# Optimization experiments

Measured on AMD Instinct MI355X. Metric: run time of the kernel, lower is better.

## Reference

```python
import jax, jax.numpy as jnp
import numpy as np

EPS = 1e-6  # cell eps
LN_EPS = 1e-5  # torch LayerNorm default


def layer_norm(x, gamma, beta):
    mu = jnp.mean(x, axis=-1, keepdims=True)
    var = jnp.mean(jnp.square(x - mu), axis=-1, keepdims=True)
    return (x - mu) * jax.lax.rsqrt(var + LN_EPS) * gamma + beta


def normalized_exp_gate(pre):
    centered = pre - jnp.mean(pre, axis=1, keepdims=True)
    e = jnp.exp(jnp.clip(centered, -5.0, 5.0))
    return e / (jnp.sum(e, axis=1, keepdims=True) + EPS)


def setup_inputs() -> dict:
    key = jax.random.key(0)
    B, Din, H = 8192, 512, 1024
    ks = jax.random.split(key, 16)
    std = 1.0 / np.sqrt(H)
    u = lambda k, shape: jax.random.uniform(k, shape, jnp.float32, -std, std)
    return {
        "x": jax.random.normal(ks[0], (B, Din), jnp.float32),
        "h_prev": jax.random.normal(ks[1], (B, H), jnp.float32),
        "c_prev": jax.random.normal(ks[2], (B, H), jnp.float32),
        "Wx": u(ks[3], (4 * H, Din)),
        "bx": u(ks[4], (4 * H,)),
        "Wh": u(ks[5], (4 * H, H)),
        "bh": u(ks[6], (4 * H,)),
        "ln_in_g": u(ks[7], (4 * H,)),
        "ln_in_b": u(ks[8], (4 * H,)),
        "ln_hu_g": u(ks[9], (4 * H,)),
        "ln_hu_b": u(ks[10], (4 * H,)),
        "ln_c_g": u(ks[11], (H,)),
        "ln_c_b": u(ks[12], (H,)),
        "ln_h_g": u(ks[13], (H,)),
        "ln_h_b": u(ks[14], (H,)),
    }


def reference(x, h_prev, c_prev, Wx, bx, Wh, bh,
              ln_in_g, ln_in_b, ln_hu_g, ln_hu_b,
              ln_c_g, ln_c_b, ln_h_g, ln_h_b):
    # dropout p=0 -> identity (eval mode)
    gates_x = layer_norm(x @ Wx.T + bx, ln_in_g, ln_in_b)      # [B, 4H]
    gates_h = layer_norm(h_prev @ Wh.T + bh, ln_hu_g, ln_hu_b)  # [B, 4H]
    gates = gates_x + gates_h
    i, f, g, o = jnp.split(gates, 4, axis=1)
    i = normalized_exp_gate(i)
    f = normalized_exp_gate(f)
    gate_sum = i + f
    i = i / (gate_sum + EPS)
    f = f / (gate_sum + EPS)
    c_tilde = jnp.tanh(g)
    c = layer_norm(f * c_prev + i * c_tilde, ln_c_g, ln_c_b)
    o = jax.nn.sigmoid(o)
    c_out = layer_norm(jnp.tanh(c), ln_h_g, ln_h_b)
    h = o * c_out
    return (h, c)
```

## Files before the change

### kernel.cpp

```cpp
#include <hip/hip_runtime.h>
#include <hip/hip_bf16.h>
#include <stdint.h>
#include <math.h>

#define EPS_CELL 1e-6f
#define LN_EPS   1e-5f

typedef short short8 __attribute__((ext_vector_type(8)));
typedef float f32x4 __attribute__((ext_vector_type(4)));
typedef unsigned short ushort;

__device__ __forceinline__ ushort f2bf(float f) {
    union { float f; uint32_t u; } v; v.f = f;
    uint32_t r = v.u + 0x7FFFu + ((v.u >> 16) & 1u);
    return (ushort)(r >> 16);
}
__device__ __forceinline__ float bfbits2f(uint32_t hi16_in_place) {
    union { uint32_t u; float f; } v; v.u = hi16_in_place;
    return v.f;
}

__device__ __forceinline__ float fexp(float x)  { return __builtin_amdgcn_exp2f(x * 1.4426950408889634f); }
__device__ __forceinline__ float frcp(float x)  { return __builtin_amdgcn_rcpf(x); }
__device__ __forceinline__ float frsq(float x)  { return __builtin_amdgcn_rsqf(x); }
__device__ __forceinline__ float ftanh(float x) {
    float xc = fminf(fmaxf(x, -15.f), 15.f);
    float t  = fexp(2.f * xc);
    return (t - 1.f) * frcp(t + 1.f);
}
__device__ __forceinline__ float fsigm(float x) { return frcp(1.f + fexp(-x)); }

__global__ __launch_bounds__(256) void cast_f32_bf16(const float* __restrict__ in,
                                                     ushort* __restrict__ out,
                                                     int n) {
    int i = (blockIdx.x * 256 + threadIdx.x) * 8;
    if (i >= n) return;
    const float4* p = (const float4*)(in + i);
    float4 a = p[0], b = p[1];
    uint4 r;
    r.x = (uint32_t)f2bf(a.x) | ((uint32_t)f2bf(a.y) << 16);
    r.y = (uint32_t)f2bf(a.z) | ((uint32_t)f2bf(a.w) << 16);
    r.z = (uint32_t)f2bf(b.x) | ((uint32_t)f2bf(b.y) << 16);
    r.w = (uint32_t)f2bf(b.z) | ((uint32_t)f2bf(b.w) << 16);
    *(uint4*)(out + i) = r;
}

#define BAR()        __builtin_amdgcn_s_barrier()
#define SPRIO(x)     __builtin_amdgcn_s_setprio(x)
#define WAIT_LGKM0() do { asm volatile("s_waitcnt lgkmcnt(0)" ::: "memory"); \
                          __builtin_amdgcn_sched_barrier(0); } while (0)
#define WAIT_VM4()   do { asm volatile("s_waitcnt vmcnt(4)" ::: "memory"); \
                          __builtin_amdgcn_sched_barrier(0); } while (0)
#define WAIT_VM0()   do { asm volatile("s_waitcnt vmcnt(0)" ::: "memory"); \
                          __builtin_amdgcn_sched_barrier(0); } while (0)

template<int K>
__global__ __launch_bounds__(512, 2) void gemm256_8ph(
        const ushort* __restrict__ Ag,
        const ushort* __restrict__ Bg,
        const float*  __restrict__ bias,
        ushort* __restrict__ C,
        int M, int GN) {
    constexpr int NT = K / 64;
    constexpr int NP = NT / 2;

    __shared__ ushort lds[65536];

    const int t    = threadIdx.x;
    const int lane = t & 63;
    const int w    = t >> 6;
    const int wr   = w >> 2;
    const int wc   = w & 3;
    const int ln   = lane & 15;
    const int hi   = lane >> 4;
    const int sx   = ln & 7;

    const int bid = blockIdx.x;
    const int wg  = (bid & 7) * 64 + (bid >> 3);
    const int n0  = (wg & 15) * 256;
    const int m0  = (wg >> 4) * 256;

    const int trow = t >> 3;
    const int scol = (((t & 7) ^ (trow & 7)) * 8);

#define STG_A(buf, j, kb) __builtin_amdgcn_global_load_lds( \
    (const __attribute__((address_space(1))) void*)(Ag + (size_t)(m0 + (j)*64 + trow) * K + (kb) + scol), \
    (__attribute__((address_space(3))) void*)(lds + (buf)*32768 + (j)*4096 + t*8), 16, 0, 0)
#define STG_B(buf, j, kb) __builtin_amdgcn_global_load_lds( \
    (const __attribute__((address_space(1))) void*)(Bg + (size_t)(n0 + (j)*64 + trow) * K + (kb) + scol), \
    (__attribute__((address_space(3))) void*)(lds + (buf)*32768 + 16384 + (j)*4096 + t*8), 16, 0, 0)

    const int ca0  = ((0 + hi) ^ sx) * 8;
    const int ca1  = ((4 + hi) ^ sx) * 8;
    const int arow = (wr * 128 + ln) * 64;
    const int brow = (wc * 64 + ln) * 64;

    short8 af[2][4], bf0[2][2], bf1[2][2];
    f32x4  acc[8][4] = {};

#define LD_A(buf, mbase) do { _Pragma("unroll") for (int m = 0; m < 4; ++m) { \
    af[0][m] = *(const short8*)&lds[(buf)*32768 + arow + ((mbase)+m)*1024 + ca0]; \
    af[1][m] = *(const short8*)&lds[(buf)*32768 + arow + ((mbase)+m)*1024 + ca1]; } } while (0)
#define LD_B(dst, buf, nbase) do { _Pragma("unroll") for (int n = 0; n < 2; ++n) { \
    dst[0][n] = *(const short8*)&lds[(buf)*32768 + 16384 + brow + ((nbase)+n)*1024 + ca0]; \
    dst[1][n] = *(const short8*)&lds[(buf)*32768 + 16384 + brow + ((nbase)+n)*1024 + ca1]; } } while (0)
#define MMQ(mb, nb, B_) do { _Pragma("unroll") for (int kk = 0; kk < 2; ++kk) \
    _Pragma("unroll") for (int m = 0; m < 4; ++m) \
    _Pragma("unroll") for (int n = 0; n < 2; ++n) \
        acc[(mb)+m][(nb)+n] = __builtin_amdgcn_mfma_f32_16x16x32_bf16( \
            af[kk][m], B_[kk][n], acc[(mb)+m][(nb)+n], 0, 0, 0); } while (0)

    STG_B(0,0,0); STG_B(0,1,0); STG_B(0,2,0); STG_B(0,3,0);
    STG_A(0,0,0); STG_A(0,1,0); STG_A(0,2,0); STG_A(0,3,0);
    STG_B(1,0,64); STG_B(1,1,64); STG_B(1,2,64); STG_B(1,3,64);
    WAIT_VM4(); BAR();

    for (int p = 0; p < NP; ++p) {
        const int k1 = (2*p + 1) * 64;
        const int t2 = (2*p + 2 < NT) ? (2*p + 2) : (2*p);
        const int t3 = (2*p + 3 < NT) ? (2*p + 3) : (2*p + 1);
        const int k2 = t2 * 64, k3 = t3 * 64;

        LD_A(0, 0); LD_B(bf0, 0, 0);
        STG_A(1,0,k1); STG_A(1,1,k1); STG_A(1,2,k1); STG_A(1,3,k1);
        BAR(); WAIT_LGKM0();
        SPRIO(1); MMQ(0,0,bf0); SPRIO(0); BAR();
        LD_B(bf1, 0, 2);
        BAR(); WAIT_LGKM0();
        SPRIO(1); MMQ(0,2,bf1); SPRIO(0); BAR();
        LD_A(0, 4);
        BAR(); WAIT_LGKM0();
        SPRIO(1); MMQ(4,0,bf0); SPRIO(0); BAR();
        STG_B(0,0,k2); STG_B(0,1,k2); STG_B(0,2,k2); STG_B(0,3,k2);
        BAR();
        SPRIO(1); MMQ(4,2,bf1); SPRIO(0);
        WAIT_VM4(); BAR();
        LD_A(1, 0); LD_B(bf0, 1, 0);
        STG_A(0,0,k2); STG_A(0,1,k2); STG_A(0,2,k2); STG_A(0,3,k2);
        BAR(); WAIT_LGKM0();
        SPRIO(1); MMQ(0,0,bf0); SPRIO(0); BAR();
        LD_B(bf1, 1, 2);
        BAR(); WAIT_LGKM0();
        SPRIO(1); MMQ(0,2,bf1); SPRIO(0); BAR();
        LD_A(1, 4);
        BAR(); WAIT_LGKM0();
        SPRIO(1); MMQ(4,0,bf0); SPRIO(0); BAR();
        STG_B(1,0,k3); STG_B(1,1,k3); STG_B(1,2,k3); STG_B(1,3,k3);
        BAR();
        SPRIO(1); MMQ(4,2,bf1); SPRIO(0);
        WAIT_VM4(); BAR();
    }

    WAIT_VM0();
    BAR();
#pragma unroll
    for (int n = 0; n < 4; ++n) {
        int cl   = wc * 64 + n * 16 + ln;
        float bv = bias[n0 + cl];
#pragma unroll
        for (int m = 0; m < 8; ++m) {
#pragma unroll
            for (int r = 0; r < 4; ++r) {
                int row = wr * 128 + m * 16 + hi * 4 + r;
                int sc  = (cl & 7) + ((((cl >> 3) ^ (row & 7))) << 3);
                lds[row * 256 + sc] = f2bf(acc[m][n][r] + bv);
            }
        }
    }
    BAR();
    {
        const int rr = t >> 5;
        const int oc = (t & 31) * 8;
#pragma unroll
        for (int i = 0; i < 16; ++i) {
            int row = i * 16 + rr;
            int sc  = (((oc >> 3) ^ (row & 7)) << 3);
            uint4 vv = *(const uint4*)&lds[row * 256 + sc];
            *(uint4*)(C + (size_t)(m0 + row) * GN + n0 + oc) = vv;
        }
    }
#undef STG_A
#undef STG_B
#undef LD_A
#undef LD_B
#undef MMQ
}

template<int NV>
__device__ __forceinline__ void block_reduce_sum(float* v, float* sred) {
    const int lane = threadIdx.x & 63;
    const int w    = threadIdx.x >> 6;
#pragma unroll
    for (int i = 0; i < NV; ++i) {
        float s = v[i];
#pragma unroll
        for (int o = 32; o > 0; o >>= 1) s += __shfl_down(s, o, 64);
        if (lane == 0) sred[i * 4 + w] = s;
    }
    __syncthreads();
#pragma unroll
    for (int i = 0; i < NV; ++i)
        v[i] = sred[i * 4 + 0] + sred[i * 4 + 1] + sred[i * 4 + 2] + sred[i * 4 + 3];
    __syncthreads();
}

__global__ __launch_bounds__(256) void fused_cell(
        const ushort* __restrict__ U, const ushort* __restrict__ V,
        const float* __restrict__ c_prev,
        const float* __restrict__ g_in, const float* __restrict__ b_in,
        const float* __restrict__ g_hu, const float* __restrict__ b_hu,
        const float* __restrict__ g_c,  const float* __restrict__ b_c,
        const float* __restrict__ g_h,  const float* __restrict__ b_h,
        float* __restrict__ out_h, float* __restrict__ out_c) {
    __shared__ float sred[16];
    const int r = blockIdx.x;
    const int t = threadIdx.x;
    const size_t rowG = (size_t)r * 4096;
    const size_t rowH = (size_t)r * 1024;
    const int c0 = t * 4;

    float uq[4][4], vq[4][4];
#pragma unroll
    for (int q = 0; q < 4; ++q) {
        uint2 uu = *(const uint2*)(U + rowG + q * 1024 + c0);
        uint2 vv = *(const uint2*)(V + rowG + q * 1024 + c0);
        uq[q][0] = bfbits2f(uu.x << 16); uq[q][1] = bfbits2f(uu.x & 0xFFFF0000u);
        uq[q][2] = bfbits2f(uu.y << 16); uq[q][3] = bfbits2f(uu.y & 0xFFFF0000u);
        vq[q][0] = bfbits2f(vv.x << 16); vq[q][1] = bfbits2f(vv.x & 0xFFFF0000u);
        vq[q][2] = bfbits2f(vv.y << 16); vq[q][3] = bfbits2f(vv.y & 0xFFFF0000u);
    }

    float red[4] = {0.f, 0.f, 0.f, 0.f};
#pragma unroll
    for (int q = 0; q < 4; ++q)
#pragma unroll
        for (int j = 0; j < 4; ++j) {
            red[0] += uq[q][j]; red[1] += uq[q][j] * uq[q][j];
            red[2] += vq[q][j]; red[3] += vq[q][j] * vq[q][j];
        }
    block_reduce_sum<4>(red, sred);
    const float inv4096 = 1.f / 4096.f;
    float mu_u = red[0] * inv4096, mu_v = red[2] * inv4096;
    float rs_u = frsq(red[1] * inv4096 - mu_u * mu_u + LN_EPS);
    float rs_v = frsq(red[3] * inv4096 - mu_v * mu_v + LN_EPS);

    float gate[4][4];
#pragma unroll
    for (int q = 0; q < 4; ++q) {
        int idx = q * 1024 + c0;
        float4 gi_ = *(const float4*)(g_in + idx);
        float4 bi_ = *(const float4*)(b_in + idx);
        float4 gh_ = *(const float4*)(g_hu + idx);
        float4 bh_ = *(const float4*)(b_hu + idx);
        float gia[4] = {gi_.x, gi_.y, gi_.z, gi_.w};
        float bia[4] = {bi_.x, bi_.y, bi_.z, bi_.w};
        float gha[4] = {gh_.x, gh_.y, gh_.z, gh_.w};
        float bha[4] = {bh_.x, bh_.y, bh_.z, bh_.w};
#pragma unroll
        for (int j = 0; j < 4; ++j) {
            float zu = (uq[q][j] - mu_u) * rs_u;
            float zv = (vq[q][j] - mu_v) * rs_v;
            gate[q][j] = zu * gia[j] + bia[j] + zv * gha[j] + bha[j];
        }
    }

    red[0] = gate[0][0] + gate[0][1] + gate[0][2] + gate[0][3];
    red[1] = gate[1][0] + gate[1][1] + gate[1][2] + gate[1][3];
    block_reduce_sum<2>(red, sred);
    const float inv1024 = 1.f / 1024.f;
    float mi = red[0] * inv1024, mf = red[1] * inv1024;

    float ei[4], ef[4];
#pragma unroll
    for (int q = 0; q < 4; ++q) {
        ei[q] = fexp(fminf(fmaxf(gate[0][q] - mi, -5.f), 5.f));
        ef[q] = fexp(fminf(fmaxf(gate[1][q] - mf, -5.f), 5.f));
    }
    red[0] = ei[0] + ei[1] + ei[2] + ei[3];
    red[1] = ef[0] + ef[1] + ef[2] + ef[3];
    block_reduce_sum<2>(red, sred);
    float inv_si = frcp(red[0] + EPS_CELL);
    float inv_sf = frcp(red[1] + EPS_CELL);

    float4 cp4 = *(const float4*)(c_prev + rowH + c0);
    float cprev[4] = {cp4.x, cp4.y, cp4.z, cp4.w};

    float cpv[4];
#pragma unroll
    for (int q = 0; q < 4; ++q) {
        float in_ = ei[q] * inv_si;
        float fn_ = ef[q] * inv_sf;
        float den = frcp(in_ + fn_ + EPS_CELL);
        float i2 = in_ * den, f2 = fn_ * den;
        cpv[q] = f2 * cprev[q] + i2 * ftanh(gate[2][q]);
    }
    red[0] = cpv[0] + cpv[1] + cpv[2] + cpv[3];
    red[1] = cpv[0] * cpv[0] + cpv[1] * cpv[1] + cpv[2] * cpv[2] + cpv[3] * cpv[3];
    block_reduce_sum<2>(red, sred);
    float mu_c = red[0] * inv1024;
    float rs_c = frsq(red[1] * inv1024 - mu_c * mu_c + LN_EPS);

    float cv[4], th[4];
    {
        float4 gc4 = *(const float4*)(g_c + c0);
        float4 bc4 = *(const float4*)(b_c + c0);
        float gca[4] = {gc4.x, gc4.y, gc4.z, gc4.w};
        float bca[4] = {bc4.x, bc4.y, bc4.z, bc4.w};
#pragma unroll
        for (int q = 0; q < 4; ++q) {
            cv[q] = (cpv[q] - mu_c) * rs_c * gca[q] + bca[q];
            th[q] = ftanh(cv[q]);
        }
    }
    {
        float4 o; o.x = cv[0]; o.y = cv[1]; o.z = cv[2]; o.w = cv[3];
        *(float4*)(out_c + rowH + c0) = o;
    }
    red[0] = th[0] + th[1] + th[2] + th[3];
    red[1] = th[0] * th[0] + th[1] * th[1] + th[2] * th[2] + th[3] * th[3];
    block_reduce_sum<2>(red, sred);
    float mu_t = red[0] * inv1024;
    float rs_t = frsq(red[1] * inv1024 - mu_t * mu_t + LN_EPS);

    float hv[4];
    {
        float4 gh4 = *(const float4*)(g_h + c0);
        float4 bh4 = *(const float4*)(b_h + c0);
        float gha[4] = {gh4.x, gh4.y, gh4.z, gh4.w};
        float bha[4] = {bh4.x, bh4.y, bh4.z, bh4.w};
#pragma unroll
        for (int q = 0; q < 4; ++q) {
            float co = (th[q] - mu_t) * rs_t * gha[q] + bha[q];
            float so = fsigm(gate[3][q]);
            hv[q] = so * co;
        }
    }
    {
        float4 o; o.x = hv[0]; o.y = hv[1]; o.z = hv[2]; o.w = hv[3];
        *(float4*)(out_h + rowH + c0) = o;
    }
}

extern "C" void kernel_launch(void* const* d_in, const int* in_sizes, int n_in,
                              void* d_out, int out_size, void* d_ws, size_t ws_size,
                              hipStream_t stream) {
    const float* x       = (const float*)d_in[0];
    const float* h_prev  = (const float*)d_in[1];
    const float* c_prev  = (const float*)d_in[2];
    const float* Wx      = (const float*)d_in[3];
    const float* bx      = (const float*)d_in[4];
    const float* Wh      = (const float*)d_in[5];
    const float* bh      = (const float*)d_in[6];
    const float* ln_in_g = (const float*)d_in[7];
    const float* ln_in_b = (const float*)d_in[8];
    const float* ln_hu_g = (const float*)d_in[9];
    const float* ln_hu_b = (const float*)d_in[10];
    const float* ln_c_g  = (const float*)d_in[11];
    const float* ln_c_b  = (const float*)d_in[12];
    const float* ln_h_g  = (const float*)d_in[13];
    const float* ln_h_b  = (const float*)d_in[14];

    const int B = 8192, Din = 512, H = 1024, G = 4096;

    ushort* xb  = (ushort*)d_ws;
    ushort* hb  = xb  + (size_t)B * Din;
    ushort* wxb = hb  + (size_t)B * H;
    ushort* whb = wxb + (size_t)G * Din;
    ushort* U   = whb + (size_t)G * H;
    ushort* V   = U   + (size_t)B * G;

    cast_f32_bf16<<<(B * Din) / 2048, 256, 0, stream>>>(x, xb, B * Din);
    cast_f32_bf16<<<(B * H)   / 2048, 256, 0, stream>>>(h_prev, hb, B * H);
    cast_f32_bf16<<<(G * Din) / 2048, 256, 0, stream>>>(Wx, wxb, G * Din);
    cast_f32_bf16<<<(G * H)   / 2048, 256, 0, stream>>>(Wh, whb, G * H);

    gemm256_8ph<512> <<<dim3(512), 512, 0, stream>>>(xb, wxb, bx, U, B, G);
    gemm256_8ph<1024><<<dim3(512), 512, 0, stream>>>(hb, whb, bh, V, B, G);

    float* out_h = (float*)d_out;
    float* out_c = out_h + (size_t)B * H;
    fused_cell<<<B, 256, 0, stream>>>(U, V, c_prev,
                                      ln_in_g, ln_in_b, ln_hu_g, ln_hu_b,
                                      ln_c_g, ln_c_b, ln_h_g, ln_h_b,
                                      out_h, out_c);
}
```

Measured before the change: 224.1 us.

## Interleave warp tile ownership and spread LDS staging loads across GEMM phases

Reassigns each wave's output sub-tiles from contiguous blocks to interleaved 16-row and 16-column strips, so each 64-row staged chunk is consumed by all waves in the first half of a k-step. That ordering lets the next tile's A and B global-to-LDS loads be split into pairs issued earlier, across several MFMA phases, instead of bursts of four. The vmcnt wait threshold rises from 4 to 6 to match the new number of in-flight loads. The goal is better overlap of global memory traffic with MFMA work, at the cost of a more fragile hazard schedule where any miscount of outstanding loads could read stale LDS.

```diff
diff --git a/kernel.cpp b/kernel.cpp
--- a/kernel.cpp
+++ b/kernel.cpp
@@ -49,7 +49,7 @@
 #define SPRIO(x)     __builtin_amdgcn_s_setprio(x)
 #define WAIT_LGKM0() do { asm volatile("s_waitcnt lgkmcnt(0)" ::: "memory"); \
                           __builtin_amdgcn_sched_barrier(0); } while (0)
-#define WAIT_VM4()   do { asm volatile("s_waitcnt vmcnt(4)" ::: "memory"); \
+#define WAIT_VM6()   do { asm volatile("s_waitcnt vmcnt(6)" ::: "memory"); \
                           __builtin_amdgcn_sched_barrier(0); } while (0)
 #define WAIT_VM0()   do { asm volatile("s_waitcnt vmcnt(0)" ::: "memory"); \
                           __builtin_amdgcn_sched_barrier(0); } while (0)
@@ -92,28 +92,32 @@
 
     const int ca0  = ((0 + hi) ^ sx) * 8;
     const int ca1  = ((4 + hi) ^ sx) * 8;
-    const int arow = (wr * 128 + ln) * 64;
-    const int brow = (wc * 64 + ln) * 64;
+    const int arow = (wr * 16 + ln) * 64;
+    const int brow = (wc * 16 + ln) * 64 + 16384;
 
     short8 af[2][4], bf0[2][2], bf1[2][2];
     f32x4  acc[8][4] = {};
 
 #define LD_A(buf, mbase) do { _Pragma("unroll") for (int m = 0; m < 4; ++m) { \
-    af[0][m] = *(const short8*)&lds[(buf)*32768 + arow + ((mbase)+m)*1024 + ca0]; \
-    af[1][m] = *(const short8*)&lds[(buf)*32768 + arow + ((mbase)+m)*1024 + ca1]; } } while (0)
+    af[0][m] = *(const short8*)&lds[(buf)*32768 + arow + ((mbase)+m)*2048 + ca0]; \
+    af[1][m] = *(const short8*)&lds[(buf)*32768 + arow + ((mbase)+m)*2048 + ca1]; } } while (0)
 #define LD_B(dst, buf, nbase) do { _Pragma("unroll") for (int n = 0; n < 2; ++n) { \
-    dst[0][n] = *(const short8*)&lds[(buf)*32768 + 16384 + brow + ((nbase)+n)*1024 + ca0]; \
-    dst[1][n] = *(const short8*)&lds[(buf)*32768 + 16384 + brow + ((nbase)+n)*1024 + ca1]; } } while (0)
+    dst[0][n] = *(const short8*)&lds[(buf)*32768 + brow + ((nbase)+n)*4096 + ca0]; \
+    dst[1][n] = *(const short8*)&lds[(buf)*32768 + brow + ((nbase)+n)*4096 + ca1]; } } while (0)
 #define MMQ(mb, nb, B_) do { _Pragma("unroll") for (int kk = 0; kk < 2; ++kk) \
     _Pragma("unroll") for (int m = 0; m < 4; ++m) \
     _Pragma("unroll") for (int n = 0; n < 2; ++n) \
         acc[(mb)+m][(nb)+n] = __builtin_amdgcn_mfma_f32_16x16x32_bf16( \
             af[kk][m], B_[kk][n], acc[(mb)+m][(nb)+n], 0, 0, 0); } while (0)
 
-    STG_B(0,0,0); STG_B(0,1,0); STG_B(0,2,0); STG_B(0,3,0);
-    STG_A(0,0,0); STG_A(0,1,0); STG_A(0,2,0); STG_A(0,3,0);
-    STG_B(1,0,64); STG_B(1,1,64); STG_B(1,2,64); STG_B(1,3,64);
-    WAIT_VM4(); BAR();
+    STG_B(0,0,0);  STG_B(0,1,0);
+    STG_A(0,0,0);  STG_A(0,1,0);
+    STG_B(0,2,0);  STG_B(0,3,0);
+    STG_A(0,2,0);  STG_A(0,3,0);
+    STG_B(1,0,64); STG_B(1,1,64);
+    STG_A(1,0,64); STG_A(1,1,64);
+    STG_B(1,2,64); STG_B(1,3,64);
+    WAIT_VM6(); BAR();
 
     for (int p = 0; p < NP; ++p) {
         const int k1 = (2*p + 1) * 64;
@@ -122,46 +126,50 @@
         const int k2 = t2 * 64, k3 = t3 * 64;
 
         LD_A(0, 0); LD_B(bf0, 0, 0);
-        STG_A(1,0,k1); STG_A(1,1,k1); STG_A(1,2,k1); STG_A(1,3,k1);
+        STG_A(1,2,k1); STG_A(1,3,k1);
         BAR(); WAIT_LGKM0();
         SPRIO(1); MMQ(0,0,bf0); SPRIO(0); BAR();
         LD_B(bf1, 0, 2);
+        STG_B(0,0,k2); STG_B(0,1,k2);
         BAR(); WAIT_LGKM0();
         SPRIO(1); MMQ(0,2,bf1); SPRIO(0); BAR();
         LD_A(0, 4);
+        STG_A(0,0,k2); STG_A(0,1,k2);
         BAR(); WAIT_LGKM0();
         SPRIO(1); MMQ(4,0,bf0); SPRIO(0); BAR();
-        STG_B(0,0,k2); STG_B(0,1,k2); STG_B(0,2,k2); STG_B(0,3,k2);
+        STG_B(0,2,k2); STG_B(0,3,k2);
         BAR();
         SPRIO(1); MMQ(4,2,bf1); SPRIO(0);
-        WAIT_VM4(); BAR();
+        WAIT_VM6(); BAR();
         LD_A(1, 0); LD_B(bf0, 1, 0);
-        STG_A(0,0,k2); STG_A(0,1,k2); STG_A(0,2,k2); STG_A(0,3,k2);
+        STG_A(0,2,k2); STG_A(0,3,k2);
         BAR(); WAIT_LGKM0();
         SPRIO(1); MMQ(0,0,bf0); SPRIO(0); BAR();
         LD_B(bf1, 1, 2);
+        STG_B(1,0,k3); STG_B(1,1,k3);
         BAR(); WAIT_LGKM0();
         SPRIO(1); MMQ(0,2,bf1); SPRIO(0); BAR();
         LD_A(1, 4);
+        STG_A(1,0,k3); STG_A(1,1,k3);
         BAR(); WAIT_LGKM0();
         SPRIO(1); MMQ(4,0,bf0); SPRIO(0); BAR();
-        STG_B(1,0,k3); STG_B(1,1,k3); STG_B(1,2,k3); STG_B(1,3,k3);
+        STG_B(1,2,k3); STG_B(1,3,k3);
         BAR();
         SPRIO(1); MMQ(4,2,bf1); SPRIO(0);
-        WAIT_VM4(); BAR();
+        WAIT_VM6(); BAR();
     }
 
     WAIT_VM0();
     BAR();
 #pragma unroll
     for (int n = 0; n < 4; ++n) {
-        int cl   = wc * 64 + n * 16 + ln;
+        int cl   = n * 64 + wc * 16 + ln;
         float bv = bias[n0 + cl];
 #pragma unroll
         for (int m = 0; m < 8; ++m) {
 #pragma unroll
             for (int r = 0; r < 4; ++r) {
-                int row = wr * 128 + m * 16 + hi * 4 + r;
+                int row = m * 32 + wr * 16 + hi * 4 + r;
                 int sc  = (cl & 7) + ((((cl >> 3) ^ (row & 7))) << 3);
                 lds[row * 256 + sc] = f2bf(acc[m][n][r] + bv);
             }
```

New measurement: 226.9 us. No clear change (+1.2%).
